# Kernel optimization log

Measured on AMD Instinct MI355X. Metric: run time of the kernel, lower is better.

Reference implementation:

```python
import jax, jax.numpy as jnp
import numpy as np

SCALE = 0.125          # feature stride 8
OUT = 7                # roi_align output size
SR = 2                 # sampling_ratio
BBW = (10.0, 10.0, 5.0, 5.0)   # torchvision BoxCoder weights
CLAMP = float(np.log(1000.0 / 16.0))
IMG_H, IMG_W = 800.0, 1088.0


def _bilinear(img, ys, xs):
    # img [C,H,W]; ys,xs [P] -> [C,P]
    C, H, W = img.shape
    y = jnp.clip(ys, 0.0, H - 1.0)
    x = jnp.clip(xs, 0.0, W - 1.0)
    y0 = jnp.floor(y); x0 = jnp.floor(x)
    y0i = y0.astype(jnp.int32); x0i = x0.astype(jnp.int32)
    y1i = jnp.minimum(y0i + 1, H - 1); x1i = jnp.minimum(x0i + 1, W - 1)
    ly = y - y0; lx = x - x0
    flat = img.reshape(C, H * W)
    g = lambda yi, xi: flat[:, yi * W + xi]
    return (g(y0i, x0i) * (1 - ly) * (1 - lx) + g(y0i, x1i) * (1 - ly) * lx
            + g(y1i, x0i) * ly * (1 - lx) + g(y1i, x1i) * ly * lx)


def _roi_align(features, boxes, roi_batch):
    # features [B,C,H,W], boxes [N,4] (image coords), roi_batch [N] -> [N,C,7,7]
    B, C, H, W = features.shape
    P = OUT * SR

    def one(b, box):
        x1, y1, x2, y2 = box[0] * SCALE, box[1] * SCALE, box[2] * SCALE, box[3] * SCALE
        rw = jnp.maximum(x2 - x1, 1.0)
        rh = jnp.maximum(y2 - y1, 1.0)
        bw = rw / OUT; bh = rh / OUT
        off = (jnp.arange(OUT)[:, None] + (jnp.arange(SR)[None, :] + 0.5) / SR).reshape(-1)  # [P]
        ys = y1 + off * bh
        xs = x1 + off * bw
        yy = jnp.repeat(ys, P)   # [P*P], y-major
        xx = jnp.tile(xs, P)
        v = _bilinear(features[b], yy, xx)                   # [C, P*P]
        return v.reshape(C, OUT, SR, OUT, SR).mean(axis=(2, 4))  # avg over samples

    return jax.vmap(one)(roi_batch, boxes)


def _decode(deltas, boxes):
    # deltas [N,K,4], boxes [N,4] -> [N,K,4]
    pw = boxes[:, 2] - boxes[:, 0]
    ph = boxes[:, 3] - boxes[:, 1]
    cx = boxes[:, 0] + 0.5 * pw
    cy = boxes[:, 1] + 0.5 * ph
    dx = deltas[..., 0] / BBW[0]; dy = deltas[..., 1] / BBW[1]
    dw = jnp.minimum(deltas[..., 2] / BBW[2], CLAMP)
    dh = jnp.minimum(deltas[..., 3] / BBW[3], CLAMP)
    pcx = dx * pw[:, None] + cx[:, None]
    pcy = dy * ph[:, None] + cy[:, None]
    pww = jnp.exp(dw) * pw[:, None]
    phh = jnp.exp(dh) * ph[:, None]
    out = jnp.stack([
        jnp.clip(pcx - 0.5 * pww, 0.0, IMG_W),
        jnp.clip(pcy - 0.5 * phh, 0.0, IMG_H),
        jnp.clip(pcx + 0.5 * pww, 0.0, IMG_W),
        jnp.clip(pcy + 0.5 * phh, 0.0, IMG_H),
    ], axis=-1)
    return out


def setup_inputs() -> dict:
    key = jax.random.key(0)
    ks = jax.random.split(key, 12)
    B, C, H, W, N, NC = 2, 256, 100, 136, 1000, 2
    features = jax.random.normal(ks[0], (B, C, H, W), jnp.float32)
    # valid proposal boxes in image coords
    cx = jax.random.uniform(ks[1], (N,)) * IMG_W
    cy = jax.random.uniform(ks[2], (N,)) * IMG_H
    bw = jax.random.uniform(ks[3], (N,)) * 240.0 + 16.0
    bh = jax.random.uniform(ks[4], (N,)) * 240.0 + 16.0
    x1 = jnp.clip(cx - 0.5 * bw, 0.0, IMG_W - 2.0)
    y1 = jnp.clip(cy - 0.5 * bh, 0.0, IMG_H - 2.0)
    x2 = jnp.clip(x1 + bw, x1 + 1.0, IMG_W - 1.0)
    y2 = jnp.clip(y1 + bh, y1 + 1.0, IMG_H - 1.0)
    boxes = jnp.stack([x1, y1, x2, y2], axis=-1).astype(jnp.float32)
    roi_batch = jax.random.randint(ks[5], (N,), 0, B, dtype=jnp.int32)
    D = C * OUT * OUT  # 12544
    HID = 1024
    s = 0.02
    fc1_w = jax.random.normal(ks[6], (D, HID), jnp.float32) * s
    fc1_b = jnp.zeros((HID,), jnp.float32)
    fc2_w = jax.random.normal(ks[7], (HID, HID), jnp.float32) * s
    fc2_b = jnp.zeros((HID,), jnp.float32)
    cls_w = jax.random.normal(ks[8], (HID, NC), jnp.float32) * s
    cls_b = jnp.zeros((NC,), jnp.float32)
    bbox_w = jax.random.normal(ks[9], (HID, NC * 4), jnp.float32) * s
    bbox_b = jnp.zeros((NC * 4,), jnp.float32)
    return {"features": features, "boxes": boxes, "roi_batch": roi_batch,
            "fc1_w": fc1_w, "fc1_b": fc1_b, "fc2_w": fc2_w, "fc2_b": fc2_b,
            "cls_w": cls_w, "cls_b": cls_b, "bbox_w": bbox_w, "bbox_b": bbox_b}


def reference(features, boxes, roi_batch, fc1_w, fc1_b, fc2_w, fc2_b, cls_w, cls_b, bbox_w, bbox_b):
    N = boxes.shape[0]
    feats = _roi_align(features, boxes, roi_batch).reshape(N, -1)  # [N, 12544]
    h = jax.nn.relu(feats @ fc1_w + fc1_b)                         # TwoMLPHead fc6
    h = jax.nn.relu(h @ fc2_w + fc2_b)                             # TwoMLPHead fc7
    scores = jax.nn.softmax(h @ cls_w + cls_b, axis=-1)            # [N, 2]
    deltas = (h @ bbox_w + bbox_b).reshape(N, -1, 4)               # [N, 2, 4]
    dec = _decode(deltas, boxes).reshape(N, -1)                    # [N, 8]
    return jnp.concatenate([dec, scores], axis=-1)                 # [N, 10]
```

## Files before the change

kernel.cpp:

```cpp
#include <hip/hip_runtime.h>
#include <hip/hip_bf16.h>

#define BF16 __hip_bfloat16

typedef __bf16 bf16x8 __attribute__((ext_vector_type(8)));
typedef float floatx4 __attribute__((ext_vector_type(4)));
typedef int intx4 __attribute__((ext_vector_type(4)));

__global__ __launch_bounds__(256) void transpose_all(const float* __restrict__ features,
                                                     const float* __restrict__ fc1_w,
                                                     const float* __restrict__ fc2_w,
                                                     BF16* __restrict__ featT,
                                                     BF16* __restrict__ w1t,
                                                     BF16* __restrict__ w2t) {
    __shared__ float tile[32][33];
    int bid = blockIdx.x;
    const float* ip;
    BF16* op;
    int R, C, cx, cy;
    if (bid < 6800) {
        int z = bid / 3400, r = bid - z * 3400;
        cx = r % 425; cy = r / 425;
        R = 256; C = 13600;
        ip = features + (size_t)z * 256 * 13600;
        op = featT + (size_t)z * 256 * 13600;
    } else if (bid < 19344) {
        int r = bid - 6800;
        cx = r & 31; cy = r >> 5;
        R = 12544; C = 1024;
        ip = fc1_w; op = w1t;
    } else {
        int r = bid - 19344;
        cx = r & 31; cy = r >> 5;
        R = 1024; C = 1024;
        ip = fc2_w; op = w2t;
    }
    int tx = threadIdx.x & 31, ty = threadIdx.x >> 5;
    int r0 = cy << 5, c0 = cx << 5;
#pragma unroll
    for (int i = 0; i < 4; ++i)
        tile[ty + i * 8][tx] = ip[(size_t)(r0 + ty + i * 8) * C + c0 + tx];
    __syncthreads();
#pragma unroll
    for (int i = 0; i < 4; ++i)
        op[(size_t)(c0 + ty + i * 8) * R + r0 + tx] = __float2bfloat16(tile[tx][ty + i * 8]);
}

__global__ __launch_bounds__(256) void roi_align_k(const BF16* __restrict__ featT,
                                                   const float* __restrict__ boxes,
                                                   const int* __restrict__ roi_batch,
                                                   BF16* __restrict__ feats) {
    __shared__ __align__(16) int   s_off[196][4];
    __shared__ __align__(16) float s_w[196][4];
    __shared__ BF16 lbuf[12544];
    int roi = blockIdx.x;
    int t = threadIdx.x;
    BF16* orow = feats + (size_t)roi * 12544;
    if (roi >= 1000) {
        uint4* o4 = (uint4*)orow;
        uint4 z = {0u, 0u, 0u, 0u};
        for (int i = t; i < 1568; i += 256) o4[i] = z;
        return;
    }
    int b = roi_batch[roi];

    if (t < 196) {
        float x1 = boxes[roi * 4 + 0] * 0.125f;
        float y1 = boxes[roi * 4 + 1] * 0.125f;
        float x2 = boxes[roi * 4 + 2] * 0.125f;
        float y2 = boxes[roi * 4 + 3] * 0.125f;
        float bw = fmaxf(x2 - x1, 1.0f) * (1.0f / 7.0f);
        float bh = fmaxf(y2 - y1, 1.0f) * (1.0f / 7.0f);
        int cell = t >> 2, s = t & 3;
        int oy = cell / 7, ox = cell - oy * 7;
        int sy = s >> 1, sx = s & 1;
        float yc = y1 + ((float)oy + ((float)sy + 0.5f) * 0.5f) * bh;
        float xc = x1 + ((float)ox + ((float)sx + 0.5f) * 0.5f) * bw;
        yc = fminf(fmaxf(yc, 0.0f), 99.0f);
        xc = fminf(fmaxf(xc, 0.0f), 135.0f);
        float y0f = floorf(yc), x0f = floorf(xc);
        int y0 = (int)y0f, x0 = (int)x0f;
        int y1i = min(y0 + 1, 99), x1i = min(x0 + 1, 135);
        float ly = yc - y0f, lx = xc - x0f;
        s_w[t][0] = (1.0f - ly) * (1.0f - lx) * 0.25f;
        s_w[t][1] = (1.0f - ly) * lx * 0.25f;
        s_w[t][2] = ly * (1.0f - lx) * 0.25f;
        s_w[t][3] = ly * lx * 0.25f;
        s_off[t][0] = (y0 * 136 + x0) * 256;
        s_off[t][1] = (y0 * 136 + x1i) * 256;
        s_off[t][2] = (y1i * 136 + x0) * 256;
        s_off[t][3] = (y1i * 136 + x1i) * 256;
    }
    __syncthreads();

    int cb = t & 31, g = t >> 5;
    const BF16* fb = featT + (size_t)b * (100 * 136 * 256) + cb * 8;
    int chbase = cb * 8;
    for (int cell = g; cell < 49; cell += 8) {
        float a[8];
#pragma unroll
        for (int j = 0; j < 8; ++j) a[j] = 0.0f;
#pragma unroll
        for (int s = 0; s < 4; ++s) {
            int p = cell * 4 + s;
#pragma unroll
            for (int tap = 0; tap < 4; ++tap) {
                float w = s_w[p][tap];
                bf16x8 v = *(const bf16x8*)(fb + s_off[p][tap]);
#pragma unroll
                for (int j = 0; j < 8; ++j) a[j] += w * (float)v[j];
            }
        }
#pragma unroll
        for (int j = 0; j < 8; ++j)
            lbuf[(chbase + j) * 49 + cell] = __float2bfloat16(a[j]);
    }
    __syncthreads();
    uint4* o4 = (uint4*)orow;
    const uint4* l4 = (const uint4*)lbuf;
    for (int i = t; i < 1568; i += 256) o4[i] = l4[i];
}

__global__ __launch_bounds__(256) void gemm_splitk(const BF16* __restrict__ A,
                                                   const BF16* __restrict__ Bt,
                                                   float* __restrict__ P,
                                                   int K, int chunk) {
    __shared__ char lds[2][2][16384];
    int w = threadIdx.x >> 6, l = threadIdx.x & 63;
    int wm = w & 1, wn = w >> 1;
    int tm = blockIdx.y, tn = blockIdx.x, s = blockIdx.z;
    int k0 = s * chunk;

    floatx4 acc[4][4];
#pragma unroll
    for (int i = 0; i < 4; ++i)
#pragma unroll
        for (int j = 0; j < 4; ++j) acc[i][j] = (floatx4){0.f, 0.f, 0.f, 0.f};

    const size_t strideA = (size_t)K * 2;
    int r8 = l >> 3;
    int g8 = (l & 7) ^ r8;
    const char* gA = (const char*)A + (size_t)(tm * 128 + w * 32 + r8) * strideA
                     + (size_t)k0 * 2 + (size_t)g8 * 16;
    const char* gB = (const char*)Bt + (size_t)(tn * 128 + w * 32 + r8) * strideA
                     + (size_t)k0 * 2 + (size_t)g8 * 16;
    int lw = w * 4096 + l * 16;

    int c = l & 15, q = l >> 4;
    int xa0 = ((0 * 4 + q) ^ (c & 7)) * 16;
    int xa1 = ((1 * 4 + q) ^ (c & 7)) * 16;
    int abase = (wm * 64 + c) * 128;
    int bbase = (wn * 64 + c) * 128;

    int nIter = chunk >> 6;

    intx4 pa[4], pb[4];
#pragma unroll
    for (int i = 0; i < 4; ++i) {
        pa[i] = *(const intx4*)(gA + (size_t)(i * 8) * strideA);
        pb[i] = *(const intx4*)(gB + (size_t)(i * 8) * strideA);
    }
#pragma unroll
    for (int i = 0; i < 4; ++i) {
        *(intx4*)(&lds[0][0][lw + i * 1024]) = pa[i];
        *(intx4*)(&lds[0][1][lw + i * 1024]) = pb[i];
    }
    __syncthreads();

    for (int kb = 0; kb < nIter; ++kb) {
        int cur = kb & 1;
        bool more = (kb + 1 < nIter);
        if (more) {
            size_t ko = (size_t)(kb + 1) * 128;
#pragma unroll
            for (int i = 0; i < 4; ++i) {
                pa[i] = *(const intx4*)(gA + (size_t)(i * 8) * strideA + ko);
                pb[i] = *(const intx4*)(gB + (size_t)(i * 8) * strideA + ko);
            }
        }
        const char* bufA = lds[cur][0];
        const char* bufB = lds[cur][1];
#pragma unroll
        for (int kk = 0; kk < 2; ++kk) {
            int xo = kk ? xa1 : xa0;
            bf16x8 af[4], bfr[4];
#pragma unroll
            for (int mi = 0; mi < 4; ++mi) af[mi] = *(const bf16x8*)(bufA + abase + mi * 2048 + xo);
#pragma unroll
            for (int ni = 0; ni < 4; ++ni) bfr[ni] = *(const bf16x8*)(bufB + bbase + ni * 2048 + xo);
#pragma unroll
            for (int mi = 0; mi < 4; ++mi)
#pragma unroll
                for (int ni = 0; ni < 4; ++ni)
                    acc[mi][ni] = __builtin_amdgcn_mfma_f32_16x16x32_bf16(af[mi], bfr[ni], acc[mi][ni], 0, 0, 0);
        }
        if (more) {
            char* nA = &lds[cur ^ 1][0][lw];
            char* nB = &lds[cur ^ 1][1][lw];
#pragma unroll
            for (int i = 0; i < 4; ++i) {
                *(intx4*)(nA + i * 1024) = pa[i];
                *(intx4*)(nB + i * 1024) = pb[i];
            }
        }
        __syncthreads();
    }

    size_t base = (size_t)s << 20;
#pragma unroll
    for (int mi = 0; mi < 4; ++mi) {
        int rowG = tm * 128 + wm * 64 + mi * 16 + q * 4;
#pragma unroll
        for (int ni = 0; ni < 4; ++ni) {
            int colG = tn * 128 + wn * 64 + ni * 16 + c;
#pragma unroll
            for (int r = 0; r < 4; ++r)
                P[base + (size_t)(rowG + r) * 1024 + colG] = acc[mi][ni][r];
        }
    }
}

__global__ __launch_bounds__(256) void reduce_k(const float* __restrict__ P,
                                                const float* __restrict__ bias,
                                                BF16* __restrict__ out,
                                                int S) {
    int i = blockIdx.x * 256 + threadIdx.x;
    float a = bias[i & 1023];
    for (int s = 0; s < S; ++s) a += P[((size_t)s << 20) + i];
    a = fmaxf(a, 0.0f);
    out[i] = __float2bfloat16(a);
}

__global__ __launch_bounds__(256) void head_k(const float* __restrict__ P2,
                                              const float* __restrict__ fc2_b,
                                              const float* __restrict__ cls_w,
                                              const float* __restrict__ cls_b,
                                              const float* __restrict__ bbox_w,
                                              const float* __restrict__ bbox_b,
                                              const float* __restrict__ boxes,
                                              float* __restrict__ out, int S2) {
    __shared__ float red[4][10];
    int roi = blockIdx.x;
    int t = threadIdx.x, w = t >> 6, l = t & 63;
    int k4 = t * 4;

    floatx4 h = *(const floatx4*)(fc2_b + k4);
    const float* pbase = P2 + (size_t)roi * 1024 + k4;
    for (int s = 0; s < S2; ++s) {
        floatx4 p = *(const floatx4*)(pbase + ((size_t)s << 20));
        h.x += p.x; h.y += p.y; h.z += p.z; h.w += p.w;
    }
    h.x = fmaxf(h.x, 0.f); h.y = fmaxf(h.y, 0.f); h.z = fmaxf(h.z, 0.f); h.w = fmaxf(h.w, 0.f);

    float acc[10];
#pragma unroll
    for (int j = 0; j < 10; ++j) acc[j] = 0.0f;
    floatx4 c0 = *(const floatx4*)(cls_w + k4 * 2);
    floatx4 c1 = *(const floatx4*)(cls_w + k4 * 2 + 4);
    acc[0] = h.x * c0.x + h.y * c0.z + h.z * c1.x + h.w * c1.z;
    acc[1] = h.x * c0.y + h.y * c0.w + h.z * c1.y + h.w * c1.w;
    const float* bw = bbox_w + k4 * 8;
#pragma unroll
    for (int kk = 0; kk < 4; ++kk) {
        float hv = (kk == 0) ? h.x : (kk == 1) ? h.y : (kk == 2) ? h.z : h.w;
        floatx4 b0 = *(const floatx4*)(bw + kk * 8);
        floatx4 b1 = *(const floatx4*)(bw + kk * 8 + 4);
        acc[2] += hv * b0.x; acc[3] += hv * b0.y; acc[4] += hv * b0.z; acc[5] += hv * b0.w;
        acc[6] += hv * b1.x; acc[7] += hv * b1.y; acc[8] += hv * b1.z; acc[9] += hv * b1.w;
    }
#pragma unroll
    for (int j = 0; j < 10; ++j) {
#pragma unroll
        for (int off = 32; off > 0; off >>= 1) acc[j] += __shfl_down(acc[j], off);
    }
    if (l == 0) {
#pragma unroll
        for (int j = 0; j < 10; ++j) red[w][j] = acc[j];
    }
    __syncthreads();
    if (t == 0) {
        float f[10];
#pragma unroll
        for (int j = 0; j < 10; ++j) f[j] = red[0][j] + red[1][j] + red[2][j] + red[3][j];
        float s0 = f[0] + cls_b[0], s1 = f[1] + cls_b[1];
        float m = fmaxf(s0, s1);
        float e0 = expf(s0 - m), e1 = expf(s1 - m);
        float inv = 1.0f / (e0 + e1);

        float bx1 = boxes[roi * 4 + 0], by1 = boxes[roi * 4 + 1];
        float bx2 = boxes[roi * 4 + 2], by2 = boxes[roi * 4 + 3];
        float pw = bx2 - bx1, ph = by2 - by1;
        float cx = bx1 + 0.5f * pw, cy = by1 + 0.5f * ph;
        const float CLAMPV = 4.135166556742356f;
        float* orow = out + roi * 10;
#pragma unroll
        for (int cl = 0; cl < 2; ++cl) {
            float dx = (f[2 + cl * 4 + 0] + bbox_b[cl * 4 + 0]) * 0.1f;
            float dy = (f[2 + cl * 4 + 1] + bbox_b[cl * 4 + 1]) * 0.1f;
            float dw = fminf((f[2 + cl * 4 + 2] + bbox_b[cl * 4 + 2]) * 0.2f, CLAMPV);
            float dh = fminf((f[2 + cl * 4 + 3] + bbox_b[cl * 4 + 3]) * 0.2f, CLAMPV);
            float pcx = dx * pw + cx, pcy = dy * ph + cy;
            float pww = expf(dw) * pw, phh = expf(dh) * ph;
            orow[cl * 4 + 0] = fminf(fmaxf(pcx - 0.5f * pww, 0.0f), 1088.0f);
            orow[cl * 4 + 1] = fminf(fmaxf(pcy - 0.5f * phh, 0.0f), 800.0f);
            orow[cl * 4 + 2] = fminf(fmaxf(pcx + 0.5f * pww, 0.0f), 1088.0f);
            orow[cl * 4 + 3] = fminf(fmaxf(pcy + 0.5f * phh, 0.0f), 800.0f);
        }
        orow[8] = e0 * inv;
        orow[9] = e1 * inv;
    }
}

extern "C" void kernel_launch(void* const* d_in, const int* in_sizes, int n_in,
                              void* d_out, int out_size, void* d_ws, size_t ws_size,
                              hipStream_t stream) {
    const float* features = (const float*)d_in[0];
    const float* boxes    = (const float*)d_in[1];
    const int*   roi_b    = (const int*)d_in[2];
    const float* fc1_w    = (const float*)d_in[3];
    const float* fc1_b    = (const float*)d_in[4];
    const float* fc2_w    = (const float*)d_in[5];
    const float* fc2_b    = (const float*)d_in[6];
    const float* cls_w    = (const float*)d_in[7];
    const float* cls_b    = (const float*)d_in[8];
    const float* bbox_w   = (const float*)d_in[9];
    const float* bbox_b   = (const float*)d_in[10];
    float* out = (float*)d_out;

    char* ws = (char*)d_ws;
    BF16* featT = (BF16*)(ws + 0);
    BF16* w1t   = (BF16*)(ws + 13926400);
    BF16* w2t   = (BF16*)(ws + 39616512);
    BF16* feats = (BF16*)(ws + 41713664);
    BF16* h1    = (BF16*)(ws + 67403776);
    float* P1   = (float*)(ws + 69500928);
    float* P2   = (float*)(ws + 0);

    int S1 = 7;
    int S2 = 4;

    transpose_all<<<20368, 256, 0, stream>>>(features, fc1_w, fc2_w, featT, w1t, w2t);

    roi_align_k<<<1024, 256, 0, stream>>>(featT, boxes, roi_b, feats);

    gemm_splitk<<<dim3(8, 8, S1), 256, 0, stream>>>(feats, w1t, P1, 12544, 12544 / S1);
    reduce_k<<<4096, 256, 0, stream>>>(P1, fc1_b, h1, S1);

    gemm_splitk<<<dim3(8, 8, S2), 256, 0, stream>>>(h1, w2t, P2, 1024, 1024 / S2);

    head_k<<<1000, 256, 0, stream>>>(P2, fc2_b, cls_w, cls_b, bbox_w, bbox_b, boxes, out, S2);
}
```

Measured before the change: 217.4 us.

## Use direct global-to-LDS loads in GEMM and widen transpose tiles

The split-K GEMM now streams tiles straight into LDS with global_load_lds instead of staging them through registers. This frees VGPRs and removes the explicit LDS store step after the MFMA loop. The transpose kernel now handles 64x32 tiles and writes packed pairs of bf16 values as 32-bit stores, which halves the block count and widens the output writes. The risk is correctness: the direct loads are issued into the other buffer while MFMAs read the current one, relying on the loop-end barrier and compiler-inserted waits for ordering.

```diff
diff --git a/kernel.cpp b/kernel.cpp
--- a/kernel.cpp
+++ b/kernel.cpp
@@ -5,7 +5,10 @@
 
 typedef __bf16 bf16x8 __attribute__((ext_vector_type(8)));
 typedef float floatx4 __attribute__((ext_vector_type(4)));
-typedef int intx4 __attribute__((ext_vector_type(4)));
+
+typedef const __attribute__((address_space(1))) void GV;
+typedef __attribute__((address_space(3))) void LV;
+#define GLD16(gp, lp) __builtin_amdgcn_global_load_lds((GV*)(gp), (LV*)(lp), 16, 0, 0)
 
 __global__ __launch_bounds__(256) void transpose_all(const float* __restrict__ features,
                                                      const float* __restrict__ fc1_w,
@@ -13,37 +16,43 @@
                                                      BF16* __restrict__ featT,
                                                      BF16* __restrict__ w1t,
                                                      BF16* __restrict__ w2t) {
-    __shared__ float tile[32][33];
+    __shared__ float tile[64][33];
     int bid = blockIdx.x;
     const float* ip;
     BF16* op;
     int R, C, cx, cy;
-    if (bid < 6800) {
-        int z = bid / 3400, r = bid - z * 3400;
+    if (bid < 3400) {
+        int z = bid / 1700, r = bid - z * 1700;
         cx = r % 425; cy = r / 425;
         R = 256; C = 13600;
         ip = features + (size_t)z * 256 * 13600;
         op = featT + (size_t)z * 256 * 13600;
-    } else if (bid < 19344) {
-        int r = bid - 6800;
+    } else if (bid < 9672) {
+        int r = bid - 3400;
         cx = r & 31; cy = r >> 5;
         R = 12544; C = 1024;
         ip = fc1_w; op = w1t;
     } else {
-        int r = bid - 19344;
+        int r = bid - 9672;
         cx = r & 31; cy = r >> 5;
         R = 1024; C = 1024;
         ip = fc2_w; op = w2t;
     }
     int tx = threadIdx.x & 31, ty = threadIdx.x >> 5;
-    int r0 = cy << 5, c0 = cx << 5;
-#pragma unroll
-    for (int i = 0; i < 4; ++i)
+    int r0 = cy << 6, c0 = cx << 5;
+#pragma unroll
+    for (int i = 0; i < 8; ++i)
         tile[ty + i * 8][tx] = ip[(size_t)(r0 + ty + i * 8) * C + c0 + tx];
     __syncthreads();
 #pragma unroll
-    for (int i = 0; i < 4; ++i)
-        op[(size_t)(c0 + ty + i * 8) * R + r0 + tx] = __float2bfloat16(tile[tx][ty + i * 8]);
+    for (int i = 0; i < 4; ++i) {
+        int c = ty + i * 8;
+        BF16 a = __float2bfloat16(tile[tx * 2][c]);
+        BF16 b = __float2bfloat16(tile[tx * 2 + 1][c]);
+        unsigned int pk = (unsigned int)*(unsigned short*)&a |
+                          ((unsigned int)*(unsigned short*)&b << 16);
+        *(unsigned int*)(op + (size_t)(c0 + c) * R + r0 + tx * 2) = pk;
+    }
 }
 
 __global__ __launch_bounds__(256) void roi_align_k(const BF16* __restrict__ featT,
@@ -154,28 +163,21 @@
 
     int nIter = chunk >> 6;
 
-    intx4 pa[4], pb[4];
 #pragma unroll
     for (int i = 0; i < 4; ++i) {
-        pa[i] = *(const intx4*)(gA + (size_t)(i * 8) * strideA);
-        pb[i] = *(const intx4*)(gB + (size_t)(i * 8) * strideA);
-    }
-#pragma unroll
-    for (int i = 0; i < 4; ++i) {
-        *(intx4*)(&lds[0][0][lw + i * 1024]) = pa[i];
-        *(intx4*)(&lds[0][1][lw + i * 1024]) = pb[i];
+        GLD16(gA + (size_t)(i * 8) * strideA, &lds[0][0][lw + i * 1024]);
+        GLD16(gB + (size_t)(i * 8) * strideA, &lds[0][1][lw + i * 1024]);
     }
     __syncthreads();
 
     for (int kb = 0; kb < nIter; ++kb) {
         int cur = kb & 1;
-        bool more = (kb + 1 < nIter);
-        if (more) {
+        if (kb + 1 < nIter) {
             size_t ko = (size_t)(kb + 1) * 128;
 #pragma unroll
             for (int i = 0; i < 4; ++i) {
-                pa[i] = *(const intx4*)(gA + (size_t)(i * 8) * strideA + ko);
-                pb[i] = *(const intx4*)(gB + (size_t)(i * 8) * strideA + ko);
+                GLD16(gA + (size_t)(i * 8) * strideA + ko, &lds[cur ^ 1][0][lw + i * 1024]);
+                GLD16(gB + (size_t)(i * 8) * strideA + ko, &lds[cur ^ 1][1][lw + i * 1024]);
             }
         }
         const char* bufA = lds[cur][0];
@@ -193,15 +195,6 @@
 #pragma unroll
                 for (int ni = 0; ni < 4; ++ni)
                     acc[mi][ni] = __builtin_amdgcn_mfma_f32_16x16x32_bf16(af[mi], bfr[ni], acc[mi][ni], 0, 0, 0);
-        }
-        if (more) {
-            char* nA = &lds[cur ^ 1][0][lw];
-            char* nB = &lds[cur ^ 1][1][lw];
-#pragma unroll
-            for (int i = 0; i < 4; ++i) {
-                *(intx4*)(nA + i * 1024) = pa[i];
-                *(intx4*)(nB + i * 1024) = pb[i];
-            }
         }
         __syncthreads();
     }
@@ -339,7 +332,7 @@
     int S1 = 7;
     int S2 = 4;
 
-    transpose_all<<<20368, 256, 0, stream>>>(features, fc1_w, fc2_w, featT, w1t, w2t);
+    transpose_all<<<10184, 256, 0, stream>>>(features, fc1_w, fc2_w, featT, w1t, w2t);
 
     roi_align_k<<<1024, 256, 0, stream>>>(featT, boxes, roi_b, feats);
 
```

Result: faster. 212.1 us (-2.5%).
